# Optimization experiments

Measured on AMD Instinct MI355X. Metric: run time of the kernel, lower is better.

The kernel has to match this reference:

```python
import jax, jax.numpy as jnp
import numpy as np

H = 2048   # hidden_size
L = 512    # latent_dim
B, S = 4, 2048

def setup_inputs() -> dict:
    key = jax.random.key(0)
    ks = jax.random.split(key, 13)
    def lin(k, fan_in, shape):
        bound = 1.0 / np.sqrt(fan_in)
        return jax.random.uniform(k, shape, jnp.float32, -bound, bound)
    return {
        "hidden_states": jax.random.normal(ks[0], (B, S, H), jnp.float32),
        "num_reasoning_steps": 8,
        # to_latent: Linear(H, 2L) -> ReLU -> Linear(2L, L)
        "W_enc1": lin(ks[1], H, (2 * L, H)), "b_enc1": lin(ks[2], H, (2 * L,)),
        "W_enc2": lin(ks[3], 2 * L, (L, 2 * L)), "b_enc2": lin(ks[4], 2 * L, (L,)),
        # from_latent: Linear(L, 2L) -> ReLU -> Linear(2L, H)
        "W_dec1": lin(ks[5], L, (2 * L, L)), "b_dec1": lin(ks[6], L, (2 * L,)),
        "W_dec2": lin(ks[7], 2 * L, (H, 2 * L)), "b_dec2": lin(ks[8], 2 * L, (H,)),
        # GRUCell(L, L): weight_ih/hh [3L, L], bias_ih/hh [3L]
        "w_ih": lin(ks[9], L, (3 * L, L)), "w_hh": lin(ks[10], L, (3 * L, L)),
        "b_ih": lin(ks[11], L, (3 * L,)), "b_hh": lin(ks[12], L, (3 * L,)),
    }

def _gru_cell(x, h, w_ih, w_hh, b_ih, b_hh):
    # PyTorch GRUCell semantics
    gi = x @ w_ih.T + b_ih   # [*, 3L]
    gh = h @ w_hh.T + b_hh
    i_r, i_z, i_n = jnp.split(gi, 3, axis=-1)
    h_r, h_z, h_n = jnp.split(gh, 3, axis=-1)
    r = jax.nn.sigmoid(i_r + h_r)
    z = jax.nn.sigmoid(i_z + h_z)
    n = jnp.tanh(i_n + r * h_n)
    return (1.0 - z) * n + z * h

def reference(hidden_states, num_reasoning_steps, W_enc1, b_enc1, W_enc2, b_enc2,
              W_dec1, b_dec1, W_dec2, b_dec2, w_ih, w_hh, b_ih, b_hh):
    # encode to latent
    latent = jax.nn.relu(hidden_states @ W_enc1.T + b_enc1) @ W_enc2.T + b_enc2  # [B,S,L]

    def step(lat, _):
        lat = _gru_cell(lat, lat, w_ih, w_hh, b_ih, b_hh)
        return lat, lat

    latent, traj = jax.lax.scan(step, latent, None, length=num_reasoning_steps)
    # traj: [steps, B, S, L] -> [B, S, steps, L]
    latent_trajectory = jnp.transpose(traj, (1, 2, 0, 3))
    decoded = jax.nn.relu(latent @ W_dec1.T + b_dec1) @ W_dec2.T + b_dec2  # [B,S,H]
    return decoded, latent_trajectory
```

## Files before the change

kernel.cpp:

```cpp
#include <hip/hip_runtime.h>
#include <hip/hip_bf16.h>
#include <cstdint>
#include <cstddef>

#define TOKENS   8192
#define HID      2048
#define LAT      512
#define LAT2     1024
#define GCOLS    2048
#define STEPS    8
#define DEC_ELEMS (TOKENS*HID)

typedef __attribute__((ext_vector_type(8))) __bf16 bf16x8;
typedef __attribute__((ext_vector_type(4))) float  f32x4;

__device__ __forceinline__ unsigned short f32_to_bf16_rne(float f) {
  unsigned int u = __float_as_uint(f);
  unsigned int r = (u + 0x7FFFu + ((u >> 16) & 1u)) >> 16;
  return (unsigned short)r;
}

__device__ __forceinline__ float sigmoidf_(float x) {
  if (x >= 0.f) { float e = __expf(-x); return 1.f / (1.f + e); }
  float e = __expf(x); return e / (1.f + e);
}
__device__ __forceinline__ float tanhf_(float x) {
  float ax = fabsf(x);
  float e  = __expf(-2.f * ax);
  float t  = (1.f - e) / (1.f + e);
  return copysignf(t, x);
}

__device__ __forceinline__ void gl_lds16(const void* g, void* l) {
  __builtin_amdgcn_global_load_lds(
      (const __attribute__((address_space(1))) void*)g,
      (__attribute__((address_space(3))) void*)l, 16, 0, 0);
}

__global__ void k_cast(const float* __restrict__ s, unsigned short* __restrict__ d, int n4) {
  int i = blockIdx.x * blockDim.x + threadIdx.x;
  int stride = gridDim.x * blockDim.x;
  for (; i < n4; i += stride) {
    float4 v = ((const float4*)s)[i];
    ushort4 o;
    o.x = f32_to_bf16_rne(v.x);
    o.y = f32_to_bf16_rne(v.y);
    o.z = f32_to_bf16_rne(v.z);
    o.w = f32_to_bf16_rne(v.w);
    ((ushort4*)d)[i] = o;
  }
}

__global__ void k_gru_pack(const float* __restrict__ wih, const float* __restrict__ whh,
                           const float* __restrict__ bih, const float* __restrict__ bhh,
                           unsigned short* __restrict__ Wg, float* __restrict__ biasg) {
  int gc = blockIdx.x;
  int l  = gc >> 2;
  int g  = gc & 3;
  int row = (g == 0) ? l : (g == 1) ? (512 + l) : (1024 + l);
  for (int c = threadIdx.x; c < LAT; c += blockDim.x) {
    float v;
    if (g <= 1)      v = wih[row * LAT + c] + whh[row * LAT + c];
    else if (g == 2) v = wih[row * LAT + c];
    else             v = whh[row * LAT + c];
    Wg[(size_t)gc * LAT + c] = f32_to_bf16_rne(v);
  }
  if (threadIdx.x == 0) {
    float b;
    if (g <= 1)      b = bih[row] + bhh[row];
    else if (g == 2) b = bih[row];
    else             b = bhh[row];
    biasg[gc] = b;
  }
}

#define MWG 128
#define NWG 128
#define KTILE 64

template <int EPI>
__global__ __launch_bounds__(256)
void gemm_bt(const unsigned short* __restrict__ A,
             const unsigned short* __restrict__ W,
             const float* __restrict__ bias,
             int K, int N,
             float* __restrict__ outF,
             unsigned short* __restrict__ outB,
             const float* __restrict__ hIn,
             float* __restrict__ traj,
             int step) {
  __shared__ __align__(16) char smem[2 * MWG * KTILE * 2];
  unsigned short* As = (unsigned short*)smem;
  unsigned short* Bs = As + MWG * KTILE;

  const int tid  = threadIdx.x;
  const int lane = tid & 63;
  const int wv   = tid >> 6;
  const int wr   = wv >> 1;
  const int wc   = wv & 1;
  const int m0   = blockIdx.x * MWG;
  const int n0   = blockIdx.y * NWG;

  const int lr = lane & 15;
  const int lq = lane >> 4;

  const int srow = lane >> 3;
  const int scol = (lane & 7) * 8;

  f32x4 acc[4][4];
#pragma unroll
  for (int i = 0; i < 4; ++i)
#pragma unroll
    for (int j = 0; j < 4; ++j) acc[i][j] = (f32x4){0.f, 0.f, 0.f, 0.f};

  const unsigned short* Ab = A + (size_t)m0 * K;
  const unsigned short* Wb = W + (size_t)n0 * K;

  const int KT = K / KTILE;
  for (int kt = 0; kt < KT; ++kt) {
    const int k0 = kt * KTILE;
#pragma unroll
    for (int q = 0; q < 4; ++q) {
      int row = 32 * wv + 8 * q + srow;
      gl_lds16(Ab + (size_t)row * K + k0 + scol, As + (32 * wv + 8 * q) * KTILE);
      gl_lds16(Wb + (size_t)row * K + k0 + scol, Bs + (32 * wv + 8 * q) * KTILE);
    }
    __syncthreads();
#pragma unroll
    for (int kk = 0; kk < KTILE; kk += 32) {
      bf16x8 af[4], bf[4];
#pragma unroll
      for (int i = 0; i < 4; ++i)
        af[i] = *(const bf16x8*)(As + (wr * 64 + i * 16 + lr) * KTILE + kk + lq * 8);
#pragma unroll
      for (int j = 0; j < 4; ++j)
        bf[j] = *(const bf16x8*)(Bs + (wc * 64 + j * 16 + lr) * KTILE + kk + lq * 8);
#pragma unroll
      for (int i = 0; i < 4; ++i)
#pragma unroll
        for (int j = 0; j < 4; ++j)
          acc[i][j] = __builtin_amdgcn_mfma_f32_16x16x32_bf16(af[i], bf[j], acc[i][j], 0, 0, 0);
    }
    __syncthreads();
  }

  if constexpr (EPI == 0 || EPI == 1 || EPI == 2) {
    float bj[4];
#pragma unroll
    for (int j = 0; j < 4; ++j) bj[j] = bias[n0 + wc * 64 + j * 16 + lr];
#pragma unroll
    for (int i = 0; i < 4; ++i) {
#pragma unroll
      for (int ii = 0; ii < 4; ++ii) {
        int row = m0 + wr * 64 + i * 16 + 4 * lq + ii;
#pragma unroll
        for (int j = 0; j < 4; ++j) {
          int col = n0 + wc * 64 + j * 16 + lr;
          float v = acc[i][j][ii] + bj[j];
          if constexpr (EPI == 0) {
            v = fmaxf(v, 0.f);
            outB[(size_t)row * N + col] = f32_to_bf16_rne(v);
          } else if constexpr (EPI == 1) {
            outF[(size_t)row * N + col] = v;
            outB[(size_t)row * N + col] = f32_to_bf16_rne(v);
          } else {
            outF[(size_t)row * N + col] = v;
          }
        }
      }
    }
  } else {
    float bj[4];
#pragma unroll
    for (int j = 0; j < 4; ++j) bj[j] = bias[n0 + wc * 64 + j * 16 + lr];
    float* epi = (float*)smem + wv * (16 * 64);
    const int latBase = (n0 >> 2) + wc * 16;
    for (int i = 0; i < 4; ++i) {
      __syncthreads();
#pragma unroll
      for (int j = 0; j < 4; ++j)
#pragma unroll
        for (int ii = 0; ii < 4; ++ii)
          epi[(4 * lq + ii) * 64 + j * 16 + lr] = acc[i][j][ii] + bj[j];
      __syncthreads();
#pragma unroll
      for (int rb = 0; rb < 4; ++rb) {
        int rr = lq + 4 * rb;
        int a  = lr;
        f32x4 g = *(const f32x4*)(epi + rr * 64 + a * 4);
        int token = m0 + wr * 64 + i * 16 + rr;
        int latc  = latBase + a;
        float h  = hIn[(size_t)token * LAT + latc];
        float r  = sigmoidf_(g.x);
        float z  = sigmoidf_(g.y);
        float n  = tanhf_(g.z + r * g.w);
        float hn = (1.f - z) * n + z * h;
        outF[(size_t)token * LAT + latc] = hn;
        outB[(size_t)token * LAT + latc] = f32_to_bf16_rne(hn);
        traj[(size_t)token * (STEPS * LAT) + step * LAT + latc] = hn;
      }
    }
  }
}

extern "C" void kernel_launch(void* const* d_in, const int* in_sizes, int n_in,
                              void* d_out, int out_size, void* d_ws, size_t ws_size,
                              hipStream_t stream) {
  const float* hs  = (const float*)d_in[0];
  const float* We1 = (const float*)d_in[2];
  const float* be1 = (const float*)d_in[3];
  const float* We2 = (const float*)d_in[4];
  const float* be2 = (const float*)d_in[5];
  const float* Wd1 = (const float*)d_in[6];
  const float* bd1 = (const float*)d_in[7];
  const float* Wd2 = (const float*)d_in[8];
  const float* bd2 = (const float*)d_in[9];
  const float* wih = (const float*)d_in[10];
  const float* whh = (const float*)d_in[11];
  const float* bih = (const float*)d_in[12];
  const float* bhh = (const float*)d_in[13];

  char* ws = (char*)d_ws;
  unsigned short* A0    = (unsigned short*)(ws + 0);
  unsigned short* We1b  = (unsigned short*)(ws + 33554432);
  unsigned short* We2b  = (unsigned short*)(ws + 37748736);
  unsigned short* Wd1b  = (unsigned short*)(ws + 38797312);
  unsigned short* Wd2b  = (unsigned short*)(ws + 39845888);
  unsigned short* Wg    = (unsigned short*)(ws + 44040192);
  float*          biasg = (float*)         (ws + 46137344);
  unsigned short* X1    = (unsigned short*)(ws + 46145536);
  float*          Lf0   = (float*)         (ws + 62922752);
  float*          Lf1   = (float*)         (ws + 79699968);
  unsigned short* Lb0   = (unsigned short*)(ws + 96477184);
  unsigned short* Lb1   = (unsigned short*)(ws + 104865792);
  unsigned short* X2    = A0;

  float* dec  = (float*)d_out;
  float* traj = (float*)d_out + DEC_ELEMS;

  k_cast<<<2048, 256, 0, stream>>>(hs,  A0,   TOKENS * HID / 4);
  k_cast<<<512,  256, 0, stream>>>(We1, We1b, LAT2 * HID / 4);
  k_cast<<<256,  256, 0, stream>>>(We2, We2b, LAT * LAT2 / 4);
  k_cast<<<256,  256, 0, stream>>>(Wd1, Wd1b, LAT2 * LAT / 4);
  k_cast<<<512,  256, 0, stream>>>(Wd2, Wd2b, HID * LAT2 / 4);
  k_gru_pack<<<GCOLS, 128, 0, stream>>>(wih, whh, bih, bhh, Wg, biasg);

  dim3 blk(256);
  gemm_bt<0><<<dim3(TOKENS / MWG, LAT2 / NWG), blk, 0, stream>>>(
      A0, We1b, be1, HID, LAT2, nullptr, X1, nullptr, nullptr, 0);
  gemm_bt<1><<<dim3(TOKENS / MWG, LAT / NWG), blk, 0, stream>>>(
      X1, We2b, be2, LAT2, LAT, Lf0, Lb0, nullptr, nullptr, 0);
  for (int s = 0; s < STEPS; ++s) {
    const unsigned short* lbi = (s & 1) ? Lb1 : Lb0;
    const float*          lfi = (s & 1) ? Lf1 : Lf0;
    unsigned short*       lbo = (s & 1) ? Lb0 : Lb1;
    float*                lfo = (s & 1) ? Lf0 : Lf1;
    gemm_bt<3><<<dim3(TOKENS / MWG, GCOLS / NWG), blk, 0, stream>>>(
        lbi, Wg, biasg, LAT, GCOLS, lfo, lbo, lfi, traj, s);
  }
  gemm_bt<0><<<dim3(TOKENS / MWG, LAT2 / NWG), blk, 0, stream>>>(
      Lb0, Wd1b, bd1, LAT, LAT2, nullptr, X2, nullptr, nullptr, 0);
  gemm_bt<2><<<dim3(TOKENS / MWG, HID / NWG), blk, 0, stream>>>(
      X2, Wd2b, bd2, LAT2, HID, dec, nullptr, nullptr, nullptr, 0);
}
```

Measured before the change: 496.8 us.

## Add 256x256 double-buffered LDS GEMM with phased MFMA scheduling

Introduces a new 512-thread GEMM kernel with 256x256 tiles. It double-buffers K-tiles in 128KB of LDS using direct global-to-LDS loads and XOR-swizzled addressing, and interleaves staging with four MFMA phases per half-iteration using barriers, priorities and explicit waitcnts. The kernel is used for the first encoder GEMM, the eight GRU step GEMMs and the final decoder GEMM. The GRU epilogue is reworked to use per-wave padded scratch without block-wide syncs. This aims to raise data reuse and overlap loads with math, but the grids are small (128 or 256 workgroups) and occupancy is limited by the LDS use.

```diff
diff --git a/kernel.cpp b/kernel.cpp
--- a/kernel.cpp
+++ b/kernel.cpp
@@ -144,19 +144,201 @@
     __syncthreads();
   }
 
+  float bj[4];
+#pragma unroll
+  for (int j = 0; j < 4; ++j) bj[j] = bias[n0 + wc * 64 + j * 16 + lr];
+#pragma unroll
+  for (int i = 0; i < 4; ++i) {
+#pragma unroll
+    for (int ii = 0; ii < 4; ++ii) {
+      int row = m0 + wr * 64 + i * 16 + 4 * lq + ii;
+#pragma unroll
+      for (int j = 0; j < 4; ++j) {
+        int col = n0 + wc * 64 + j * 16 + lr;
+        float v = acc[i][j][ii] + bj[j];
+        if constexpr (EPI == 0) {
+          v = fmaxf(v, 0.f);
+          outB[(size_t)row * N + col] = f32_to_bf16_rne(v);
+        } else if constexpr (EPI == 1) {
+          outF[(size_t)row * N + col] = v;
+          outB[(size_t)row * N + col] = f32_to_bf16_rne(v);
+        } else {
+          outF[(size_t)row * N + col] = v;
+        }
+      }
+    }
+  }
+}
+
+
+#define WAIT_LGKM0() asm volatile("s_waitcnt lgkmcnt(0)" ::: "memory")
+#define WAIT_VM(n)   asm volatile("s_waitcnt vmcnt(" #n ")" ::: "memory")
+
+#define LOAD_A(buf, mh) { \
+  const int baseA = (buf)*65536 + wm*16384; \
+  _Pragma("unroll") for (int m4 = 0; m4 < 4; ++m4) \
+  _Pragma("unroll") for (int kki = 0; kki < 2; ++kki) { \
+    int rl = (mh)*64 + m4*16 + lr; \
+    int off = (rl*128 + kki*64 + lq*16) ^ ((rl & 7) << 4); \
+    aR[mh][m4][kki] = *(const bf16x8*)(lds_ + baseA + off); } }
+
+#define LOAD_B(buf, nh) { \
+  const int baseB = (buf)*65536 + 32768 + (wn >> 1)*16384; \
+  _Pragma("unroll") for (int n2 = 0; n2 < 2; ++n2) \
+  _Pragma("unroll") for (int kki = 0; kki < 2; ++kki) { \
+    int rl = (wn & 1)*64 + ((nh)*2 + n2)*16 + lr; \
+    int off = (rl*128 + kki*64 + lq*16) ^ ((rl & 7) << 4); \
+    bR[nh][n2][kki] = *(const bf16x8*)(lds_ + baseB + off); } }
+
+#define STAGE_A(buf, half, kt) { \
+  const unsigned short* gp = A + (size_t)(m0 + (half)*128 + rr8)*K + (size_t)(kt)*64 + cc8; \
+  char* dp = lds_ + (buf)*65536 + (half)*16384 + (wv << 10); \
+  gl_lds16(gp, dp); \
+  gl_lds16(gp + (size_t)64*K, dp + 8192); }
+
+#define STAGE_B(buf, half, kt) { \
+  const unsigned short* gp = W + (size_t)(n0 + (half)*128 + rr8)*K + (size_t)(kt)*64 + cc8; \
+  char* dp = lds_ + (buf)*65536 + 32768 + (half)*16384 + (wv << 10); \
+  gl_lds16(gp, dp); \
+  gl_lds16(gp + (size_t)64*K, dp + 8192); }
+
+#define MFMAQ(mh, nh) \
+  _Pragma("unroll") for (int kki = 0; kki < 2; ++kki) \
+  _Pragma("unroll") for (int n2 = 0; n2 < 2; ++n2) \
+  _Pragma("unroll") for (int m4 = 0; m4 < 4; ++m4) \
+    acc[(mh)*4 + m4][(nh)*2 + n2] = __builtin_amdgcn_mfma_f32_16x16x32_bf16( \
+        aR[mh][m4][kki], bR[nh][n2][kki], acc[(mh)*4 + m4][(nh)*2 + n2], 0, 0, 0);
+
+#define PH_CORE(mh, nh) \
+  __builtin_amdgcn_s_barrier(); \
+  WAIT_LGKM0(); \
+  __builtin_amdgcn_sched_barrier(0); \
+  __builtin_amdgcn_s_setprio(1); \
+  MFMAQ(mh, nh); \
+  __builtin_amdgcn_sched_barrier(0); \
+  __builtin_amdgcn_s_setprio(0);
+
+#define PH_BAR() __builtin_amdgcn_s_barrier();
+
+template <int EPI>
+__global__ __launch_bounds__(512, 2)
+void gemm256(const unsigned short* __restrict__ A,
+             const unsigned short* __restrict__ W,
+             const float* __restrict__ bias,
+             int K, int N, int Ntiles,
+             float* __restrict__ outF,
+             unsigned short* __restrict__ outB,
+             const float* __restrict__ hIn,
+             float* __restrict__ traj,
+             int step) {
+  __shared__ __align__(16) char lds_[131072];
+
+  const int tid  = threadIdx.x;
+  const int lane = tid & 63;
+  const int wv   = tid >> 6;
+  const int wm   = wv >> 2;
+  const int wn   = wv & 3;
+  const int lr   = lane & 15;
+  const int lq   = lane >> 4;
+
+  const int rr8 = (wv << 3) + (lane >> 3);
+  const int cc8 = ((lane & 7) ^ (lane >> 3)) << 3;
+
+  {
+  }
+  const int nwg = gridDim.x;
+  const int wg  = blockIdx.x;
+  const int swz = (wg & 7) * (nwg >> 3) + (wg >> 3);
+  const int tm  = swz / Ntiles;
+  const int tn  = swz % Ntiles;
+  const int m0  = tm * 256;
+  const int n0  = tn * 256;
+
+  f32x4 acc[8][4];
+#pragma unroll
+  for (int i = 0; i < 8; ++i)
+#pragma unroll
+    for (int j = 0; j < 4; ++j) acc[i][j] = (f32x4){0.f, 0.f, 0.f, 0.f};
+
+  bf16x8 aR[2][4][2];
+  bf16x8 bR[2][2][2];
+
+  const int nIt = K >> 7;
+
+  STAGE_B(0, 0, 0) STAGE_B(0, 1, 0) STAGE_A(0, 0, 0) STAGE_A(0, 1, 0)
+  STAGE_B(1, 0, 1) STAGE_B(1, 1, 1)
+  WAIT_VM(4);
+  __builtin_amdgcn_s_barrier();
+
+  for (int t = 0; t < nIt - 1; ++t) {
+    const int kt1 = 2 * t + 1;
+    const int kt2 = 2 * t + 2;
+    const int kt3 = 2 * t + 3;
+    LOAD_A(0, 0) LOAD_B(0, 0)
+    STAGE_A(1, 0, kt1)
+    PH_CORE(0, 0) PH_BAR()
+    LOAD_B(0, 1)
+    STAGE_A(1, 1, kt1)
+    PH_CORE(0, 1) PH_BAR()
+    LOAD_A(0, 1)
+    STAGE_B(0, 0, kt2)
+    PH_CORE(1, 1) PH_BAR()
+    STAGE_B(0, 1, kt2)
+    PH_CORE(1, 0)
+    WAIT_VM(4);
+    PH_BAR()
+    LOAD_A(1, 0) LOAD_B(1, 0)
+    STAGE_A(0, 0, kt2)
+    PH_CORE(0, 0) PH_BAR()
+    LOAD_B(1, 1)
+    STAGE_A(0, 1, kt2)
+    PH_CORE(0, 1) PH_BAR()
+    LOAD_A(1, 1)
+    STAGE_B(1, 0, kt3)
+    PH_CORE(1, 1) PH_BAR()
+    STAGE_B(1, 1, kt3)
+    PH_CORE(1, 0)
+    WAIT_VM(4);
+    PH_BAR()
+  }
+
+  {
+    const int ktL = 2 * nIt - 1;
+    LOAD_A(0, 0) LOAD_B(0, 0)
+    STAGE_A(1, 0, ktL)
+    PH_CORE(0, 0) PH_BAR()
+    LOAD_B(0, 1)
+    STAGE_A(1, 1, ktL)
+    PH_CORE(0, 1) PH_BAR()
+    LOAD_A(0, 1)
+    PH_CORE(1, 1) PH_BAR()
+    PH_CORE(1, 0)
+    WAIT_VM(0);
+    PH_BAR()
+    LOAD_A(1, 0) LOAD_B(1, 0)
+    PH_CORE(0, 0) PH_BAR()
+    LOAD_B(1, 1)
+    PH_CORE(0, 1) PH_BAR()
+    LOAD_A(1, 1)
+    PH_CORE(1, 1) PH_BAR()
+    PH_CORE(1, 0)
+    PH_BAR()
+  }
+
+  float bj[4];
+#pragma unroll
+  for (int nf = 0; nf < 4; ++nf) bj[nf] = bias[n0 + wn * 64 + nf * 16 + lr];
+
   if constexpr (EPI == 0 || EPI == 1 || EPI == 2) {
-    float bj[4];
-#pragma unroll
-    for (int j = 0; j < 4; ++j) bj[j] = bias[n0 + wc * 64 + j * 16 + lr];
-#pragma unroll
-    for (int i = 0; i < 4; ++i) {
+#pragma unroll
+    for (int mf = 0; mf < 8; ++mf) {
 #pragma unroll
       for (int ii = 0; ii < 4; ++ii) {
-        int row = m0 + wr * 64 + i * 16 + 4 * lq + ii;
-#pragma unroll
-        for (int j = 0; j < 4; ++j) {
-          int col = n0 + wc * 64 + j * 16 + lr;
-          float v = acc[i][j][ii] + bj[j];
+        int row = m0 + wm * 128 + mf * 16 + lq * 4 + ii;
+#pragma unroll
+        for (int nf = 0; nf < 4; ++nf) {
+          int col = n0 + wn * 64 + nf * 16 + lr;
+          float v = acc[mf][nf][ii] + bj[nf];
           if constexpr (EPI == 0) {
             v = fmaxf(v, 0.f);
             outB[(size_t)row * N + col] = f32_to_bf16_rne(v);
@@ -170,26 +352,25 @@
       }
     }
   } else {
-    float bj[4];
-#pragma unroll
-    for (int j = 0; j < 4; ++j) bj[j] = bias[n0 + wc * 64 + j * 16 + lr];
-    float* epi = (float*)smem + wv * (16 * 64);
-    const int latBase = (n0 >> 2) + wc * 16;
-    for (int i = 0; i < 4; ++i) {
-      __syncthreads();
-#pragma unroll
-      for (int j = 0; j < 4; ++j)
+    float* scr = (float*)lds_ + wv * 1088;
+    const int latBase = tn * 64 + wn * 16;
+    const int la = lane & 15;
+    const int th = lane >> 4;
+#pragma unroll
+    for (int mf = 0; mf < 8; ++mf) {
+      WAIT_LGKM0();
+#pragma unroll
+      for (int nf = 0; nf < 4; ++nf)
 #pragma unroll
         for (int ii = 0; ii < 4; ++ii)
-          epi[(4 * lq + ii) * 64 + j * 16 + lr] = acc[i][j][ii] + bj[j];
-      __syncthreads();
-#pragma unroll
-      for (int rb = 0; rb < 4; ++rb) {
-        int rr = lq + 4 * rb;
-        int a  = lr;
-        f32x4 g = *(const f32x4*)(epi + rr * 64 + a * 4);
-        int token = m0 + wr * 64 + i * 16 + rr;
-        int latc  = latBase + a;
+          scr[(lq * 4 + ii) * 68 + nf * 16 + lr] = acc[mf][nf][ii] + bj[nf];
+      WAIT_LGKM0();
+#pragma unroll
+      for (int tb = 0; tb < 4; ++tb) {
+        int tt = th * 4 + tb;
+        int token = m0 + wm * 128 + mf * 16 + tt;
+        f32x4 g = *(const f32x4*)(scr + tt * 68 + la * 4);
+        int latc = latBase + la;
         float h  = hIn[(size_t)token * LAT + latc];
         float r  = sigmoidf_(g.x);
         float z  = sigmoidf_(g.y);
@@ -245,21 +426,20 @@
   k_cast<<<512,  256, 0, stream>>>(Wd2, Wd2b, HID * LAT2 / 4);
   k_gru_pack<<<GCOLS, 128, 0, stream>>>(wih, whh, bih, bhh, Wg, biasg);
 
-  dim3 blk(256);
-  gemm_bt<0><<<dim3(TOKENS / MWG, LAT2 / NWG), blk, 0, stream>>>(
-      A0, We1b, be1, HID, LAT2, nullptr, X1, nullptr, nullptr, 0);
-  gemm_bt<1><<<dim3(TOKENS / MWG, LAT / NWG), blk, 0, stream>>>(
+  gemm256<0><<<128, 512, 0, stream>>>(A0, We1b, be1, HID, LAT2, 4,
+                                      nullptr, X1, nullptr, nullptr, 0);
+  gemm_bt<1><<<dim3(TOKENS / MWG, LAT / NWG), dim3(256), 0, stream>>>(
       X1, We2b, be2, LAT2, LAT, Lf0, Lb0, nullptr, nullptr, 0);
   for (int s = 0; s < STEPS; ++s) {
     const unsigned short* lbi = (s & 1) ? Lb1 : Lb0;
     const float*          lfi = (s & 1) ? Lf1 : Lf0;
     unsigned short*       lbo = (s & 1) ? Lb0 : Lb1;
     float*                lfo = (s & 1) ? Lf0 : Lf1;
-    gemm_bt<3><<<dim3(TOKENS / MWG, GCOLS / NWG), blk, 0, stream>>>(
-        lbi, Wg, biasg, LAT, GCOLS, lfo, lbo, lfi, traj, s);
-  }
-  gemm_bt<0><<<dim3(TOKENS / MWG, LAT2 / NWG), blk, 0, stream>>>(
+    gemm256<3><<<256, 512, 0, stream>>>(lbi, Wg, biasg, LAT, GCOLS, 8,
+                                        lfo, lbo, lfi, traj, s);
+  }
+  gemm_bt<0><<<dim3(TOKENS / MWG, LAT2 / NWG), dim3(256), 0, stream>>>(
       Lb0, Wd1b, bd1, LAT, LAT2, nullptr, X2, nullptr, nullptr, 0);
-  gemm_bt<2><<<dim3(TOKENS / MWG, HID / NWG), blk, 0, stream>>>(
-      X2, Wd2b, bd2, LAT2, HID, dec, nullptr, nullptr, nullptr, 0);
-}
+  gemm256<2><<<256, 512, 0, stream>>>(X2, Wd2b, bd2, LAT2, HID, 8,
+                                      dec, nullptr, nullptr, nullptr, 0);
+}
```

Result: faster. 463.3 us (-6.7%).
